# Optimization experiments

Hardware: AMD Instinct MI355X
Metric: run time of the kernel (lower is better)

The kernel has to match this reference:

```python
import jax, jax.numpy as jnp
import numpy as np

H, W, D = 160, 160, 16
VOXEL_SIZE = 0.4
VOL_MIN = np.array([-32.0, -32.0, -1.0], dtype=np.float32)
SCALE_MULTIPLIER = 3.0
N_GAUSS = 8192
CHUNK = 64


def setup_inputs() -> dict:
    key = jax.random.key(0)
    k1, k2, k3, k4, k5 = jax.random.split(key, 5)
    vol_min = jnp.asarray(VOL_MIN)
    vol_ext = jnp.array([64.0, 64.0, 6.4], dtype=jnp.float32)
    means3d = jax.random.uniform(k1, (N_GAUSS, 3), jnp.float32) * vol_ext + vol_min
    opacities = jax.random.uniform(k2, (N_GAUSS, 1), jnp.float32)
    # per-axis std devs: 0.2..0.8 m so 3-sigma footprint spans a handful of voxels
    scales = 0.2 + 0.6 * jax.random.uniform(k3, (N_GAUSS, 3), jnp.float32)
    rotations = jax.random.normal(k4, (N_GAUSS, 4), jnp.float32)
    features = jax.random.normal(k5, (N_GAUSS, 32), jnp.float32)
    return {"means3d": means3d, "opacities": opacities, "scales": scales,
            "rotations": rotations, "features": features}


def quat_to_rotmat(q):
    # q: [N,4] wxyz, normalized
    w, x, y, z = q[:, 0], q[:, 1], q[:, 2], q[:, 3]
    R = jnp.stack([
        jnp.stack([1 - 2 * (y * y + z * z), 2 * (x * y - w * z), 2 * (x * z + w * y)], -1),
        jnp.stack([2 * (x * y + w * z), 1 - 2 * (x * x + z * z), 2 * (y * z - w * x)], -1),
        jnp.stack([2 * (x * z - w * y), 2 * (y * z + w * x), 1 - 2 * (x * x + y * y)], -1),
    ], axis=-2)  # [N,3,3]
    return R


def _grid_coords():
    ii, jj, kk = jnp.meshgrid(jnp.arange(H), jnp.arange(W), jnp.arange(D), indexing="ij")
    idx = jnp.stack([ii, jj, kk], axis=-1).astype(jnp.float32)
    return (idx + 0.5) * VOXEL_SIZE + jnp.asarray(VOL_MIN)  # [H,W,D,3] voxel centers


def reference(means3d, opacities, scales, rotations, features):
    x = _grid_coords().reshape(-1, 3)  # [V,3]
    q = rotations / jnp.linalg.norm(rotations, axis=-1, keepdims=True)
    R = quat_to_rotmat(q)
    # covariance = R diag(s^2) R^T
    cov = jnp.einsum("nij,nj,nkj->nik", R, scales * scales, R)
    cov_inv = jnp.linalg.inv(cov)
    sigma = jnp.sqrt(jnp.diagonal(cov, axis1=1, axis2=2))  # [N,3]
    opac = opacities[:, 0]  # [N]
    n = means3d.shape[0]
    nchunks = n // CHUNK

    def chunked(a):
        return a.reshape(nchunks, CHUNK, *a.shape[1:])

    def step(acc, c):
        mu, op, sg, ci, ft = c
        diff = x[:, None, :] - mu[None, :, :]  # [V,CHUNK,3]
        maha = jnp.einsum("vci,cij,vcj->vc", diff, ci, diff)
        # local aggregation cutoff: within scale_multiplier * sigma box around mean
        mask = jnp.all(jnp.abs(diff) <= SCALE_MULTIPLIER * sg[None, :, :], axis=-1)
        w = op[None, :] * jnp.exp(-0.5 * maha) * mask  # [V,CHUNK]
        return acc + w @ ft, None

    acc0 = jnp.zeros((x.shape[0], features.shape[-1]), jnp.float32)
    xs = (chunked(means3d), chunked(opac), chunked(sigma), chunked(cov_inv), chunked(features))
    acc, _ = jax.lax.scan(step, acc0, xs)
    return acc.reshape(H, W, D, features.shape[-1])
```

## Files before the change

### kernel.cpp

```cpp
#include <hip/hip_runtime.h>

#define HH 160
#define WW 160
#define DD 16
#define NG 8192
#define VOXEL 0.4f

#define TTX 40
#define TTY 40
#define TTZ 4
#define NTILES (TTX * TTY * TTZ)
#define CAP 128


__global__ __launch_bounds__(64) void gv_precompute_bin(
    const float* __restrict__ means, const float* __restrict__ opac,
    const float* __restrict__ scales, const float* __restrict__ rots,
    float4* __restrict__ pack, int* __restrict__ tileCnt,
    int* __restrict__ tileList) {
  int g = blockIdx.x * 64 + threadIdx.x;
  if (g >= NG) return;
  float qw = rots[g * 4 + 0], qx = rots[g * 4 + 1];
  float qy = rots[g * 4 + 2], qz = rots[g * 4 + 3];
  float inv = rsqrtf(qw * qw + qx * qx + qy * qy + qz * qz);
  qw *= inv; qx *= inv; qy *= inv; qz *= inv;
  float R[3][3];
  R[0][0] = 1.f - 2.f * (qy * qy + qz * qz);
  R[0][1] = 2.f * (qx * qy - qw * qz);
  R[0][2] = 2.f * (qx * qz + qw * qy);
  R[1][0] = 2.f * (qx * qy + qw * qz);
  R[1][1] = 1.f - 2.f * (qx * qx + qz * qz);
  R[1][2] = 2.f * (qy * qz - qw * qx);
  R[2][0] = 2.f * (qx * qz - qw * qy);
  R[2][1] = 2.f * (qy * qz + qw * qx);
  R[2][2] = 1.f - 2.f * (qx * qx + qy * qy);
  float sx = scales[g * 3 + 0], sy = scales[g * 3 + 1], sz = scales[g * 3 + 2];
  float s2[3] = {sx * sx, sy * sy, sz * sz};
  float is2[3] = {1.f / s2[0], 1.f / s2[1], 1.f / s2[2]};
  float cov00 = 0.f, cov11 = 0.f, cov22 = 0.f;
  float ci00 = 0.f, ci01 = 0.f, ci02 = 0.f, ci11 = 0.f, ci12 = 0.f, ci22 = 0.f;
#pragma unroll
  for (int c = 0; c < 3; c++) {
    cov00 += R[0][c] * R[0][c] * s2[c];
    cov11 += R[1][c] * R[1][c] * s2[c];
    cov22 += R[2][c] * R[2][c] * s2[c];
    ci00 += R[0][c] * R[0][c] * is2[c];
    ci01 += R[0][c] * R[1][c] * is2[c];
    ci02 += R[0][c] * R[2][c] * is2[c];
    ci11 += R[1][c] * R[1][c] * is2[c];
    ci12 += R[1][c] * R[2][c] * is2[c];
    ci22 += R[2][c] * R[2][c] * is2[c];
  }
  float mx = means[g * 3 + 0], my = means[g * 3 + 1], mz = means[g * 3 + 2];
  float bx = 3.f * sqrtf(cov00), by = 3.f * sqrtf(cov11), bz = 3.f * sqrtf(cov22);
  float4* p = pack + (size_t)g * 4;
  p[0] = make_float4(mx, my, mz, opac[g]);
  p[1] = make_float4(bx, by, bz, ci00);
  p[2] = make_float4(ci01, ci02, ci11, ci12);
  p[3] = make_float4(ci22, 0.f, 0.f, 0.f);

  const float eps = 1e-4f;
  int i0 = (int)ceilf((mx - bx + 32.f) * 2.5f - 0.5f - eps);
  int i1 = (int)floorf((mx + bx + 32.f) * 2.5f - 0.5f + eps);
  int j0 = (int)ceilf((my - by + 32.f) * 2.5f - 0.5f - eps);
  int j1 = (int)floorf((my + by + 32.f) * 2.5f - 0.5f + eps);
  int k0 = (int)ceilf((mz - bz + 1.f) * 2.5f - 0.5f - eps);
  int k1 = (int)floorf((mz + bz + 1.f) * 2.5f - 0.5f + eps);
  i0 = max(i0, 0); i1 = min(i1, HH - 1);
  j0 = max(j0, 0); j1 = min(j1, WW - 1);
  k0 = max(k0, 0); k1 = min(k1, DD - 1);
  if (i0 > i1 || j0 > j1 || k0 > k1) return;
  int ti0 = i0 >> 2, ti1 = i1 >> 2;
  int tj0 = j0 >> 2, tj1 = j1 >> 2;
  int tk0 = k0 >> 2, tk1 = k1 >> 2;
  for (int ti = ti0; ti <= ti1; ti++)
    for (int tj = tj0; tj <= tj1; tj++)
      for (int tk = tk0; tk <= tk1; tk++) {
        int t = (ti * TTY + tj) * TTZ + tk;
        int pos = atomicAdd(&tileCnt[t], 1);
        if (pos < CAP) tileList[t * CAP + pos] = g;
      }
}

__global__ __launch_bounds__(128) void gv_voxelize(
    const float4* __restrict__ pack, const float4* __restrict__ feats,
    const int* __restrict__ tileCnt, const int* __restrict__ tileList,
    float4* __restrict__ out) {
  int tid = threadIdx.x;
  int lane = tid & 63;
  int wv = tid >> 6;
  int di = (lane >> 4) & 3, dj = (lane >> 2) & 3, dk = lane & 3;
  int tk = blockIdx.x * 2 + wv;
  int tj = blockIdx.y, ti = blockIdx.z;
  int i = ti * 4 + di, j = tj * 4 + dj, k = tk * 4 + dk;

  float px = (i + 0.5f) * VOXEL - 32.f;
  float py = (j + 0.5f) * VOXEL - 32.f;
  float pz = (k + 0.5f) * VOXEL - 1.f;

  int t = (ti * TTY + tj) * TTZ + tk;
  int cnt = min(tileCnt[t], CAP);
  const int* lst = tileList + t * CAP;

  float4 acc[8];
#pragma unroll
  for (int f = 0; f < 8; f++) acc[f] = make_float4(0.f, 0.f, 0.f, 0.f);

  for (int base = 0; base < cnt; base += 64) {
    int m = min(64, cnt - base);
    int lidx = lst[base + min(lane, m - 1)];

#pragma unroll 2
    for (int n = 0; n < m; n++) {
      int gg = __builtin_amdgcn_readfirstlane(__shfl(lidx, n, 64));
      const float* p = (const float*)(pack + (size_t)gg * 4);
      float mux = p[0], muy = p[1], muz = p[2], op = p[3];
      float bbx = p[4], bby = p[5], bbz = p[6], c00 = p[7];
      float c01 = p[8], c02 = p[9], c11 = p[10], c12 = p[11];
      float c22 = p[12];
      const float4* ft = feats + (size_t)gg * 8;

      float dx = px - mux, dy = py - muy, dz = pz - muz;
      bool in = (fabsf(dx) <= bbx) & (fabsf(dy) <= bby) & (fabsf(dz) <= bbz);
      float maha = c00 * dx * dx + c11 * dy * dy + c22 * dz * dz +
                   2.f * (c01 * dx * dy + c02 * dx * dz + c12 * dy * dz);
      float w = in ? op * __expf(-0.5f * maha) : 0.f;
#pragma unroll
      for (int f = 0; f < 8; f++) {
        float4 fv = ft[f];
        acc[f].x += w * fv.x;
        acc[f].y += w * fv.y;
        acc[f].z += w * fv.z;
        acc[f].w += w * fv.w;
      }
    }
  }

  size_t v = ((size_t)i * WW + j) * DD + k;
  float4* o = out + v * 8;
#pragma unroll
  for (int f = 0; f < 8; f++) o[f] = acc[f];
}

extern "C" void kernel_launch(void* const* d_in, const int* in_sizes, int n_in,
                              void* d_out, int out_size, void* d_ws, size_t ws_size,
                              hipStream_t stream) {
  const float* means  = (const float*)d_in[0];
  const float* opac   = (const float*)d_in[1];
  const float* scales = (const float*)d_in[2];
  const float* rots   = (const float*)d_in[3];
  const float4* feats = (const float4*)d_in[4];

  char* ws = (char*)d_ws;
  float4* pack   = (float4*)ws;
  int* tileCnt   = (int*)(ws + 512 * 1024);
  int* tileList  = (int*)(ws + 544 * 1024);

  hipMemsetAsync(tileCnt, 0, NTILES * sizeof(int), stream);
  gv_precompute_bin<<<NG / 64, 64, 0, stream>>>(means, opac, scales, rots,
                                                pack, tileCnt, tileList);
  dim3 grid(2, TTY, TTX);
  gv_voxelize<<<grid, 128, 0, stream>>>(pack, feats, tileCnt, tileList,
                                        (float4*)d_out);
}
```

Measured before the change: 129.4 us.

## Stage per-tile Gaussian params and features in LDS with cooperative loads

The voxelize kernel now runs one 64-thread block per tile and stages up to 32 Gaussians' packed parameters and features into shared memory. The whole wave loads them cooperatively with coalesced float4 reads, and the inner loop then reads them from LDS. Before, each Gaussian was fetched with dependent, wave-uniform scalar and vector global loads. The change adds __syncthreads barriers per batch and LDS traffic, and the grid mapping changes from 128-thread blocks to 64-thread blocks.

```diff
diff --git a/kernel.cpp b/kernel.cpp
--- a/kernel.cpp
+++ b/kernel.cpp
@@ -82,23 +82,26 @@
       }
 }
 
-__global__ __launch_bounds__(128) void gv_voxelize(
-    const float4* __restrict__ pack, const float4* __restrict__ feats,
+__global__ __launch_bounds__(64, 4) void gv_voxelize(
+    const float4* __restrict__ packv, const float4* __restrict__ featv,
     const int* __restrict__ tileCnt, const int* __restrict__ tileList,
     float4* __restrict__ out) {
-  int tid = threadIdx.x;
-  int lane = tid & 63;
-  int wv = tid >> 6;
+  __shared__ int s_gi[32];
+  __shared__ float4 s_d[32 * 12];
+
+  int lane = threadIdx.x;
+  int t = blockIdx.x;
+  int ti = t / (TTY * TTZ);
+  int rem = t - ti * (TTY * TTZ);
+  int tj = rem / TTZ;
+  int tk = rem - tj * TTZ;
   int di = (lane >> 4) & 3, dj = (lane >> 2) & 3, dk = lane & 3;
-  int tk = blockIdx.x * 2 + wv;
-  int tj = blockIdx.y, ti = blockIdx.z;
   int i = ti * 4 + di, j = tj * 4 + dj, k = tk * 4 + dk;
 
   float px = (i + 0.5f) * VOXEL - 32.f;
   float py = (j + 0.5f) * VOXEL - 32.f;
   float pz = (k + 0.5f) * VOXEL - 1.f;
 
-  int t = (ti * TTY + tj) * TTZ + tk;
   int cnt = min(tileCnt[t], CAP);
   const int* lst = tileList + t * CAP;
 
@@ -106,28 +109,37 @@
 #pragma unroll
   for (int f = 0; f < 8; f++) acc[f] = make_float4(0.f, 0.f, 0.f, 0.f);
 
-  for (int base = 0; base < cnt; base += 64) {
-    int m = min(64, cnt - base);
-    int lidx = lst[base + min(lane, m - 1)];
+  for (int base = 0; base < cnt; base += 32) {
+    int m = min(32, cnt - base);
+    __syncthreads();
+    if (lane < 32) s_gi[lane] = lst[base + min(lane, m - 1)];
+    __syncthreads();
+
+#pragma unroll
+    for (int r = 0; r < 6; r++) {
+      int idx = lane + 64 * r;
+      int s = idx / 12;
+      int piece = idx - s * 12;
+      int gg = s_gi[s];
+      const float4* src = (piece < 4)
+          ? (packv + (size_t)gg * 4 + piece)
+          : (featv + (size_t)gg * 8 + (piece - 4));
+      s_d[idx] = *src;
+    }
+    __syncthreads();
 
 #pragma unroll 2
     for (int n = 0; n < m; n++) {
-      int gg = __builtin_amdgcn_readfirstlane(__shfl(lidx, n, 64));
-      const float* p = (const float*)(pack + (size_t)gg * 4);
-      float mux = p[0], muy = p[1], muz = p[2], op = p[3];
-      float bbx = p[4], bby = p[5], bbz = p[6], c00 = p[7];
-      float c01 = p[8], c02 = p[9], c11 = p[10], c12 = p[11];
-      float c22 = p[12];
-      const float4* ft = feats + (size_t)gg * 8;
-
-      float dx = px - mux, dy = py - muy, dz = pz - muz;
-      bool in = (fabsf(dx) <= bbx) & (fabsf(dy) <= bby) & (fabsf(dz) <= bbz);
-      float maha = c00 * dx * dx + c11 * dy * dy + c22 * dz * dz +
-                   2.f * (c01 * dx * dy + c02 * dx * dz + c12 * dy * dz);
-      float w = in ? op * __expf(-0.5f * maha) : 0.f;
+      const float4* sp = s_d + n * 12;
+      float4 p0 = sp[0], p1 = sp[1], p2 = sp[2], p3 = sp[3];
+      float dx = px - p0.x, dy = py - p0.y, dz = pz - p0.z;
+      bool in = (fabsf(dx) <= p1.x) & (fabsf(dy) <= p1.y) & (fabsf(dz) <= p1.z);
+      float maha = p1.w * dx * dx + p2.z * dy * dy + p3.x * dz * dz +
+                   2.f * (p2.x * dx * dy + p2.y * dx * dz + p2.w * dy * dz);
+      float w = in ? p0.w * __expf(-0.5f * maha) : 0.f;
 #pragma unroll
       for (int f = 0; f < 8; f++) {
-        float4 fv = ft[f];
+        float4 fv = sp[4 + f];
         acc[f].x += w * fv.x;
         acc[f].y += w * fv.y;
         acc[f].z += w * fv.z;
@@ -149,7 +161,7 @@
   const float* opac   = (const float*)d_in[1];
   const float* scales = (const float*)d_in[2];
   const float* rots   = (const float*)d_in[3];
-  const float4* feats = (const float4*)d_in[4];
+  const float4* featv = (const float4*)d_in[4];
 
   char* ws = (char*)d_ws;
   float4* pack   = (float4*)ws;
@@ -159,7 +171,6 @@
   hipMemsetAsync(tileCnt, 0, NTILES * sizeof(int), stream);
   gv_precompute_bin<<<NG / 64, 64, 0, stream>>>(means, opac, scales, rots,
                                                 pack, tileCnt, tileList);
-  dim3 grid(2, TTY, TTX);
-  gv_voxelize<<<grid, 128, 0, stream>>>(pack, feats, tileCnt, tileList,
-                                        (float4*)d_out);
+  gv_voxelize<<<NTILES, 64, 0, stream>>>(pack, featv, tileCnt, tileList,
+                                         (float4*)d_out);
 }
```

After: 136.9 us. 5.8% more time.
